# Kernel tuning notes

Measured on AMD Instinct MI355X. Metric: run time of the kernel, lower is better.

## Reference

```python
import jax, jax.numpy as jnp
import numpy as np
from jax import lax

B = 4; NB = 8192; N = B * NB; C = 64; K = 32; S = 128
GRID = np.array([[4.0, 4.0, 4.0], [16.0, 16.0, 16.0], [2.0, 2.0, 2.0]], np.float32)
relu = jax.nn.relu
sig = jax.nn.sigmoid

def _bn(x, g, b):
    # BatchNorm1d, training mode (biased batch stats), eps=1e-5
    m = x.mean(0)
    v = jnp.var(x, axis=0)
    return (x - m) * lax.rsqrt(v + 1e-5) * g + b

def _seg_sum(x, seg):
    return jax.ops.segment_sum(x, seg, num_segments=N)

def _seg_mean(x, seg):
    s = _seg_sum(x, seg)
    cnt = _seg_sum(jnp.ones((x.shape[0], 1), x.dtype), seg)
    return s / jnp.maximum(cnt, 1.0)

def _knn_geom(pts):
    # pts: [NB,3]. cdist + KNN + per-point 3x3 PCA (linearity) + density.
    sq = (pts * pts).sum(-1)
    d = jnp.sqrt(jnp.maximum(sq[:, None] + sq[None, :] - 2.0 * (pts @ pts.T), 0.0))
    negd, idx = lax.top_k(-d, K + 1)
    idx = idx[:, 1:]          # drop self
    nd = -negd[:, 1:]         # neighbor distances [NB,K]
    nbr = pts[idx]            # [NB,K,3]
    cen = nbr - nbr.mean(1, keepdims=True)
    cov = jnp.einsum('nki,nkj->nij', cen, cen) / (K - 1)
    s = jnp.linalg.svd(cov, compute_uv=False)   # [NB,3] descending
    s = s / s.sum(-1, keepdims=True)
    lin = s[:, 0] - s[:, 1] - s[:, 2]
    dens = 1.0 / (nd.mean(1) + 1e-6)
    return lin, dens

def _cluster(coordf, batch, size):
    # torch_geometric voxel_grid (start = per-dim min) + unique(return_inverse)
    v = jnp.floor((coordf - coordf.min(0)) / jnp.maximum(size, 1e-6)).astype(jnp.int32)
    rows = jnp.concatenate([batch[:, None], v], axis=1)
    _, inv = jnp.unique(rows, axis=0, size=N, return_inverse=True, fill_value=0)
    return jnp.reshape(inv, (-1,))

def _subm_conv(f, W, table, coords, batch):
    # SubMConv3d 3x3x3: output only at active sites; hash-table neighbor lookup.
    out = jnp.zeros((f.shape[0], W.shape[-1]), f.dtype)
    k = 0
    for dx in (-1, 0, 1):
        for dy in (-1, 0, 1):
            for dz in (-1, 0, 1):
                nc = coords + jnp.array([dx, dy, dz], jnp.int32)
                valid = jnp.all((nc >= 0) & (nc < S), axis=1)
                ncc = jnp.clip(nc, 0, S - 1)
                nidx = table[batch, ncc[:, 0], ncc[:, 1], ncc[:, 2]]
                ok = valid & (nidx >= 0)
                nf = jnp.where(ok[:, None], f[jnp.maximum(nidx, 0)], 0.0)
                out = out + nf @ W[k]
                k += 1
    return out

def _forward(feat, cm_fp_w, cm_fp_b, cm_fp_g, cm_fp_beta, cm_ca_w1, cm_ca_b1, cm_ca_w2, cm_ca_b2, cm_na_w1, cm_na_b1, cm_na_w2, cm_na_b2, cm_ff_w1, cm_ff_b1, cm_ff_g, cm_ff_beta, cm_ff_w2, cm_ff_b2, cm_sa_w1, cm_sa_b1, cm_sa_w2, cm_sa_b2, fj_w1, fj_b1, fj_g, fj_beta, fj_w2, fj_b2, proj_w, proj_g, proj_beta, lw_w, lw_g, lw_beta, wt_w, adp_w, fuse_w, fuse_g, fuse_beta, conv1_w, bn1_g, bn1_b, conv2_w, bn2_g, bn2_b, coords, batch):
    # ---- CMPFE ----
    p = relu(_bn(feat @ cm_fp_w + cm_fp_b, cm_fp_g, cm_fp_beta))
    cf, colf, nof = p[:, 0:3], p[:, 3:6], p[:, 6:9]
    ca = sig(relu(colf @ cm_ca_w1 + cm_ca_b1) @ cm_ca_w2 + cm_ca_b2)
    na = sig(relu(nof @ cm_na_w1 + cm_na_b1) @ cm_na_w2 + cm_na_b2)
    enh = jnp.concatenate([cf, colf * ca, nof * na], axis=1)
    ff = relu(_bn(enh @ cm_ff_w1 + cm_ff_b1, cm_ff_g, cm_ff_beta)) @ cm_ff_w2 + cm_ff_b2
    sa = sig(relu(ff @ cm_sa_w1 + cm_sa_b1) @ cm_sa_w2 + cm_sa_b2)
    feat = ff * sa + feat * (1.0 - sa)

    # ---- PFAS: geometry (per scene, sequential to bound memory) ----
    coordf = coords.astype(feat.dtype)
    lin, dens = lax.map(_knn_geom, coordf.reshape(B, NB, 3))
    lin = lin.reshape(-1)
    dens = dens.reshape(-1)

    logits = relu(_bn(feat @ fj_w1 + fj_b1, fj_g, fj_beta)) @ fj_w2 + fj_b2
    probs = jax.nn.softmax(logits, axis=1)
    tower = (2.0 * dens + probs[:, 0]) / 3.0
    back = (jnp.maximum(1.0 - lin, 1.0 - dens) + probs[:, 1]) / 3.0
    line = (2.0 * lin + probs[:, 2]) / 3.0
    opts = jnp.asarray(GRID)
    lg = opts[2] * jnp.array([1.0, 1.0, 5.0], feat.dtype)  # z grid x5 for lines
    gs = tower[:, None] * opts[0] + back[:, None] * opts[1] + line[:, None] * lg + 1e-6

    # ---- representative grids (N > 200 branch) ----
    gm = gs.mean(1)
    order = jnp.argsort(gm)
    reps = [gs[order[100:200]].mean(0), gs[order[::-1][:100]].mean(0), gs[order[:100]].mean(0)]

    # ---- multi-depth cluster attention fusion ----
    feats = []
    for i in range(3):
        cl = _cluster(coordf, batch, reps[i])
        pw = relu(_bn(feat @ lw_w[i], lw_g[i], lw_beta[i]))
        pw = pw - _seg_mean(pw, cl)[cl]
        pw = pw @ wt_w[i]
        pw = jnp.exp(pw - jnp.max(pw))
        pw = pw / (_seg_sum(pw, cl)[cl] + 1e-6)
        pf = relu(_bn(feat @ proj_w[i], proj_g[i], proj_beta[i])) * pw
        feats.append(_seg_sum(pf, cl)[cl])
    adp = jax.nn.softmax(feat @ adp_w, axis=1)           # [N,3]
    fused = jnp.einsum('nc,ncd->nd', adp, jnp.stack(feats, axis=1))
    fl = relu(_bn(feat @ proj_w[3], proj_g[3], proj_beta[3]))
    h = relu(_bn(jnp.concatenate([fl, fused], axis=1) @ fuse_w, fuse_g, fuse_beta)) + feat
    res = h

    # ---- sparse voxel residual block ----
    table = jnp.full((B, S, S, S), -1, jnp.int32).at[batch, coords[:, 0], coords[:, 1], coords[:, 2]].set(jnp.arange(N, dtype=jnp.int32))
    v = relu(_bn(_subm_conv(h, conv1_w, table, coords, batch), bn1_g, bn1_b))
    v = _bn(_subm_conv(v, conv2_w, table, coords, batch), bn2_g, bn2_b)
    return relu(v + res)

def setup_inputs() -> dict:
    key = jax.random.key(0)
    ks = iter(jax.random.split(key, 80))
    rng = np.random.default_rng(0)
    cl = []
    for b in range(B):  # unique voxel coords per scene
        li = rng.choice(S ** 3, size=NB, replace=False)
        cl.append(np.stack([li // (S * S), (li // S) % S, li % S], axis=1))
    coords = jnp.asarray(np.concatenate(cl, 0), jnp.int32)
    batch = jnp.repeat(jnp.arange(B, dtype=jnp.int32), NB)

    def W(sh, fan):
        return jax.random.normal(next(ks), sh, jnp.float32) / np.sqrt(fan)

    def bias(sh):
        return 0.01 * jax.random.normal(next(ks), sh, jnp.float32)

    def gamma(sh):
        return 1.0 + 0.01 * jax.random.normal(next(ks), sh, jnp.float32)

    inp = dict(
        feat=jax.random.normal(next(ks), (N, C), jnp.float32),
        coords=coords, batch=batch,
        cm_fp_w=W((C, 9), C), cm_fp_b=bias((9,)), cm_fp_g=gamma((9,)), cm_fp_beta=bias((9,)),
        cm_ca_w1=W((3, 16), 3), cm_ca_b1=bias((16,)), cm_ca_w2=W((16, 3), 16), cm_ca_b2=bias((3,)),
        cm_na_w1=W((3, 16), 3), cm_na_b1=bias((16,)), cm_na_w2=W((16, 3), 16), cm_na_b2=bias((3,)),
        cm_ff_w1=W((9, C), 9), cm_ff_b1=bias((C,)), cm_ff_g=gamma((C,)), cm_ff_beta=bias((C,)),
        cm_ff_w2=W((C, C), C), cm_ff_b2=bias((C,)),
        cm_sa_w1=W((C, C // 2), C), cm_sa_b1=bias((C // 2,)), cm_sa_w2=W((C // 2, 1), C // 2), cm_sa_b2=bias((1,)),
        fj_w1=W((C, 64), C), fj_b1=bias((64,)), fj_g=gamma((64,)), fj_beta=bias((64,)),
        fj_w2=W((64, 3), 64), fj_b2=bias((3,)),
        proj_w=W((4, C, C), C), proj_g=gamma((4, C)), proj_beta=bias((4, C)),
        lw_w=W((3, C, C), C), lw_g=gamma((3, C)), lw_beta=bias((3, C)),
        wt_w=W((3, C, C), C), adp_w=W((C, 3), C),
        fuse_w=W((2 * C, C), 2 * C), fuse_g=gamma((C,)), fuse_beta=bias((C,)),
        conv1_w=W((27, C, C), 27 * C), bn1_g=gamma((C,)), bn1_b=bias((C,)),
        conv2_w=W((27, C, C), 27 * C), bn2_g=gamma((C,)), bn2_b=bias((C,)))
    return inp

def reference(feat, coords, batch, cm_fp_w, cm_fp_b, cm_fp_g, cm_fp_beta, cm_ca_w1, cm_ca_b1, cm_ca_w2, cm_ca_b2, cm_na_w1, cm_na_b1, cm_na_w2, cm_na_b2, cm_ff_w1, cm_ff_b1, cm_ff_g, cm_ff_beta, cm_ff_w2, cm_ff_b2, cm_sa_w1, cm_sa_b1, cm_sa_w2, cm_sa_b2, fj_w1, fj_b1, fj_g, fj_beta, fj_w2, fj_b2, proj_w, proj_g, proj_beta, lw_w, lw_g, lw_beta, wt_w, adp_w, fuse_w, fuse_g, fuse_beta, conv1_w, bn1_g, bn1_b, conv2_w, bn2_g, bn2_b):
    return _forward(feat, cm_fp_w, cm_fp_b, cm_fp_g, cm_fp_beta, cm_ca_w1, cm_ca_b1, cm_ca_w2, cm_ca_b2, cm_na_w1, cm_na_b1, cm_na_w2, cm_na_b2, cm_ff_w1, cm_ff_b1, cm_ff_g, cm_ff_beta, cm_ff_w2, cm_ff_b2, cm_sa_w1, cm_sa_b1, cm_sa_w2, cm_sa_b2, fj_w1, fj_b1, fj_g, fj_beta, fj_w2, fj_b2, proj_w, proj_g, proj_beta, lw_w, lw_g, lw_beta, wt_w, adp_w, fuse_w, fuse_g, fuse_beta, conv1_w, bn1_g, bn1_b, conv2_w, bn2_g, bn2_b, coords, batch)
```

## Files before the change

kernel.cpp:

```cpp
#include <hip/hip_runtime.h>

typedef unsigned int u32;
typedef unsigned long long u64;
typedef unsigned short u16;

#define NPTS 32768
#define NBP 8192
#define SD 128
#define KP1 33
#define NSPLIT 4
#define NROWS (NSPLIT*KP1)
#define HCAP (1u<<18)
#define MB8 8388608ULL
#define DCAP 136
#define DSTR 138
#define KCAP 57

__device__ __forceinline__ float fsig(float x){ return 1.0f/(1.0f+expf(-x)); }
__device__ __forceinline__ u32 f2o(float f){ u32 b=__float_as_uint(f); return (b&0x80000000u)? ~b : (b|0x80000000u); }
__device__ __forceinline__ float o2f(u32 o){ u32 b=(o&0x80000000u)? (o&0x7fffffffu) : ~o; return __uint_as_float(b); }
__device__ __forceinline__ u32 hashk(u64 k){
  k^=k>>33; k*=0xff51afd7ed558ccdULL; k^=k>>33; k*=0xc4ceb9fe1a85ec53ULL; k^=k>>33;
  return (u32)k;
}
__device__ __forceinline__ void bnab(const float* st,const float* g,const float* be,int c,float& A,float& B){
  float m=st[c]*(1.0f/32768.0f);
  float var=st[64+c]*(1.0f/32768.0f)-m*m;
  var=fmaxf(var,0.f);
  float a=g[c]/sqrtf(var+1e-5f);
  A=a; B=be[c]-m*a;
}

__global__ void k_initmisc(int* misc){ int t=threadIdx.x; if(t<3) misc[t]=0x7fffffff; }

__global__ __launch_bounds__(256) void k_prep(const int* coords,int* misc,int* table){
  int t=blockIdx.x*256+threadIdx.x;
  int x=coords[3*t],y=coords[3*t+1],z=coords[3*t+2];
  int mx=x,my=y,mz=z;
  for(int o=32;o>=1;o>>=1){ mx=min(mx,__shfl_down(mx,o)); my=min(my,__shfl_down(my,o)); mz=min(mz,__shfl_down(mz,o)); }
  if((threadIdx.x&63)==0){ atomicMin(&misc[0],mx); atomicMin(&misc[1],my); atomicMin(&misc[2],mz); }
  int b=t>>13;
  table[(((b<<7)|x)<<7|y)<<7|z]=t;
}

__global__ __launch_bounds__(256) void k1(const float* feat,const float* w,const float* b,float* P9,float* st0){
  __shared__ float sm[256*17];
  __shared__ float wl[576];
  __shared__ float bl[9];
  int tid=threadIdx.x; int n0=blockIdx.x*256;
  for(int i=tid;i<576;i+=256) wl[i]=w[i];
  if(tid<9) bl[tid]=b[tid];
  float acc[9];
  #pragma unroll
  for(int c=0;c<9;c++) acc[c]=0.f;
  for(int ch=0;ch<4;ch++){
    __syncthreads();
    for(int m=0;m<16;m++){
      int e=tid+256*m; int p=e>>4,c=e&15;
      sm[p*17+c]=feat[(size_t)(n0+p)*64+ch*16+c];
    }
    __syncthreads();
    for(int j=0;j<16;j++){
      float x=sm[tid*17+j];
      const float* r=&wl[(ch*16+j)*9];
      #pragma unroll
      for(int c=0;c<9;c++) acc[c]+=x*r[c];
    }
  }
  #pragma unroll
  for(int c=0;c<9;c++) acc[c]+=bl[c];
  int n=n0+tid;
  #pragma unroll
  for(int c=0;c<9;c++) P9[(size_t)n*9+c]=acc[c];
  int lane=tid&63;
  for(int c=0;c<9;c++){
    float v=acc[c],v2=v*v;
    for(int o=32;o>=1;o>>=1){ v+=__shfl_down(v,o); v2+=__shfl_down(v2,o); }
    if(lane==0){ atomicAdd(&st0[c],v); atomicAdd(&st0[64+c],v2); }
  }
}

__global__ __launch_bounds__(256) void k2(const float* P9,const float* fpg,const float* fpbe,
    const float* caw1,const float* cab1,const float* caw2,const float* cab2,
    const float* naw1,const float* nab1,const float* naw2,const float* nab2,
    const float* ffw1,const float* ffb1,const float* st0,float* T1,float* st1){
  __shared__ float A0[9],B0[9];
  __shared__ float cw1[48],cb1[16],cw2[48],cb2[3];
  __shared__ float nw1[48],nb1[16],nw2[48],nb2[3];
  __shared__ float fw[576],fb[64];
  __shared__ float redS[256],redQ[256];
  int tid=threadIdx.x;
  if(tid<9){
    float m=st0[tid]*(1.0f/32768.0f);
    float var=st0[64+tid]*(1.0f/32768.0f)-m*m;
    var=fmaxf(var,0.f);
    float a=fpg[tid]/sqrtf(var+1e-5f);
    A0[tid]=a; B0[tid]=fpbe[tid]-m*a;
  }
  for(int i=tid;i<48;i+=256){ cw1[i]=caw1[i]; cw2[i]=caw2[i]; nw1[i]=naw1[i]; nw2[i]=naw2[i]; }
  if(tid<16){ cb1[tid]=cab1[tid]; nb1[tid]=nab1[tid]; }
  if(tid<3){ cb2[tid]=cab2[tid]; nb2[tid]=nab2[tid]; }
  for(int i=tid;i<576;i+=256) fw[i]=ffw1[i];
  if(tid<64) fb[tid]=ffb1[tid];
  __syncthreads();
  int n=blockIdx.x*256+tid;
  float p[9];
  #pragma unroll
  for(int c=0;c<9;c++){ float x=P9[(size_t)n*9+c]; p[c]=fmaxf(x*A0[c]+B0[c],0.f); }
  float ca[3],na[3];
  {
    float h[16];
    #pragma unroll
    for(int hh=0;hh<16;hh++){ float s=cb1[hh];
      #pragma unroll
      for(int c=0;c<3;c++) s+=p[3+c]*cw1[c*16+hh];
      h[hh]=fmaxf(s,0.f); }
    #pragma unroll
    for(int o=0;o<3;o++){ float s=cb2[o];
      #pragma unroll
      for(int hh=0;hh<16;hh++) s+=h[hh]*cw2[hh*3+o];
      ca[o]=fsig(s); }
  }
  {
    float h[16];
    #pragma unroll
    for(int hh=0;hh<16;hh++){ float s=nb1[hh];
      #pragma unroll
      for(int c=0;c<3;c++) s+=p[6+c]*nw1[c*16+hh];
      h[hh]=fmaxf(s,0.f); }
    #pragma unroll
    for(int o=0;o<3;o++){ float s=nb2[o];
      #pragma unroll
      for(int hh=0;hh<16;hh++) s+=h[hh]*nw2[hh*3+o];
      na[o]=fsig(s); }
  }
  float enh[9]={p[0],p[1],p[2],p[3]*ca[0],p[4]*ca[1],p[5]*ca[2],p[6]*na[0],p[7]*na[1],p[8]*na[2]};
  float acc[64];
  #pragma unroll
  for(int co=0;co<64;co++) acc[co]=fb[co];
  #pragma unroll
  for(int c=0;c<9;c++){ float x=enh[c]; const float* r=&fw[c*64];
    #pragma unroll
    for(int co=0;co<64;co++) acc[co]+=x*r[co]; }
  float4* o4=(float4*)&T1[(size_t)n*64];
  #pragma unroll
  for(int q=0;q<16;q++) o4[q]=make_float4(acc[4*q],acc[4*q+1],acc[4*q+2],acc[4*q+3]);
  int lane=tid&63, wv=tid>>6;
  for(int c=0;c<64;c++){
    float v=acc[c],v2=v*v;
    for(int o=32;o>=1;o>>=1){ v+=__shfl_down(v,o); v2+=__shfl_down(v2,o); }
    if(lane==0){ redS[wv*64+c]=v; redQ[wv*64+c]=v2; }
  }
  __syncthreads();
  if(tid<64){
    float a=0,b2=0;
    for(int w=0;w<4;w++){ a+=redS[w*64+tid]; b2+=redQ[w*64+tid]; }
    atomicAdd(&st1[tid],a); atomicAdd(&st1[64+tid],b2);
  }
}

__global__ __launch_bounds__(256) void k3(const float* T1,const float* feat,float* FF,float* T2,
    const float* st1,const float* ffg,const float* ffbe,
    const float* w2,const float* b2,
    const float* saw1,const float* sab1,const float* saw2,const float* sab2,
    const float* fjw1,const float* fjb1,float* st2){
  __shared__ float it[64*65];
  __shared__ float wt[4096];
  __shared__ float wsa[2048];
  __shared__ float red[2048];
  __shared__ float sb1[32],sw2[32],sav[64];
  __shared__ float A1[64],B1[64];
  __shared__ float sb2s;
  int tid=threadIdx.x; int n0=blockIdx.x*64;
  if(tid<64){ float A,B; bnab(st1,ffg,ffbe,tid,A,B); A1[tid]=A; B1[tid]=B; }
  for(int m=0;m<16;m++){ int i=tid+256*m; wt[i]=w2[i]; }
  for(int i=tid;i<2048;i+=256) wsa[i]=saw1[i];
  if(tid<32){ sb1[tid]=sab1[tid]; sw2[tid]=saw2[tid]; }
  if(tid==0) sb2s=sab2[0];
  __syncthreads();
  for(int m=0;m<16;m++){
    int e=tid+256*m; int p=e>>6,c=e&63;
    float x=T1[(size_t)n0*64+e];
    it[p*65+c]=fmaxf(x*A1[c]+B1[c],0.f);
  }
  __syncthreads();
  int tx4=tid&15, ty=tid>>4;
  float acc[4][4];
  #pragma unroll
  for(int j=0;j<4;j++){
    #pragma unroll
    for(int q=0;q<4;q++) acc[j][q]=0.f;
  }
  for(int ci=0;ci<64;ci++){
    float4 w4=*(float4*)&wt[ci*64+tx4*4];
    #pragma unroll
    for(int j=0;j<4;j++){
      float x=it[(ty+16*j)*65+ci];
      acc[j][0]+=x*w4.x; acc[j][1]+=x*w4.y; acc[j][2]+=x*w4.z; acc[j][3]+=x*w4.w;
    }
  }
  float bb[4];
  #pragma unroll
  for(int q=0;q<4;q++) bb[q]=b2[tx4*4+q];
  __syncthreads();
  #pragma unroll
  for(int j=0;j<4;j++){
    #pragma unroll
    for(int q=0;q<4;q++) it[(ty+16*j)*65+tx4*4+q]=acc[j][q]+bb[q];
  }
  __syncthreads();
  if(tid<64){
    float s1[32];
    #pragma unroll
    for(int h=0;h<32;h++) s1[h]=sb1[h];
    for(int ci=0;ci<64;ci++){
      float x=it[tid*65+ci];
      #pragma unroll
      for(int h=0;h<32;h++) s1[h]+=x*wsa[ci*32+h];
    }
    float s=sb2s;
    #pragma unroll
    for(int h=0;h<32;h++) s+=fmaxf(s1[h],0.f)*sw2[h];
    sav[tid]=fsig(s);
  }
  __syncthreads();
  for(int m=0;m<16;m++){
    int e=tid+256*m; int p=e>>6,c=e&63;
    float ffv=it[p*65+c]; float sv=sav[p];
    float fn=ffv*sv+feat[(size_t)n0*64+e]*(1.0f-sv);
    FF[(size_t)n0*64+e]=fn;
    it[p*65+c]=fn;
  }
  __syncthreads();
  for(int m=0;m<16;m++){ int i=tid+256*m; wt[i]=fjw1[i]; }
  __syncthreads();
  float ac2[4][4];
  #pragma unroll
  for(int j=0;j<4;j++){
    #pragma unroll
    for(int q=0;q<4;q++) ac2[j][q]=0.f;
  }
  for(int ci=0;ci<64;ci++){
    float4 w4=*(float4*)&wt[ci*64+tx4*4];
    #pragma unroll
    for(int j=0;j<4;j++){
      float x=it[(ty+16*j)*65+ci];
      ac2[j][0]+=x*w4.x; ac2[j][1]+=x*w4.y; ac2[j][2]+=x*w4.z; ac2[j][3]+=x*w4.w;
    }
  }
  float fjb[4];
  #pragma unroll
  for(int q=0;q<4;q++) fjb[q]=fjb1[tx4*4+q];
  #pragma unroll
  for(int j=0;j<4;j++){
    #pragma unroll
    for(int q=0;q<4;q++) ac2[j][q]+=fjb[q];
    *(float4*)&T2[(size_t)(n0+ty+16*j)*64+tx4*4]=make_float4(ac2[j][0],ac2[j][1],ac2[j][2],ac2[j][3]);
  }
  #pragma unroll
  for(int q=0;q<4;q++){
    float s=0,s2=0;
    #pragma unroll
    for(int j=0;j<4;j++){ s+=ac2[j][q]; s2+=ac2[j][q]*ac2[j][q]; }
    red[ty*64+tx4*4+q]=s; red[1024+ty*64+tx4*4+q]=s2;
  }
  __syncthreads();
  if(tid<64){
    float a=0,b3=0;
    for(int t=0;t<16;t++){ a+=red[t*64+tid]; b3+=red[1024+t*64+tid]; }
    atomicAdd(&st2[tid],a); atomicAdd(&st2[64+tid],b3);
  }
}

__global__ __launch_bounds__(256) void k4(const float* T2,const float* FF,const float* st2,
    const float* fjg,const float* fjbe,const float* fjw2,const float* fjb2,
    const float* adpw,float* PROBS,float* ADP){
  __shared__ float t2t[64*65],fft[64*65];
  __shared__ float A2[64],B2[64];
  __shared__ float w2l[192],b2l[3],awl[192];
  int tid=threadIdx.x; int n0=blockIdx.x*64;
  if(tid<64){ float A,B; bnab(st2,fjg,fjbe,tid,A,B); A2[tid]=A; B2[tid]=B; }
  for(int i=tid;i<192;i+=256){ w2l[i]=fjw2[i]; awl[i]=adpw[i]; }
  if(tid<3) b2l[tid]=fjb2[tid];
  for(int m=0;m<16;m++){
    int e=tid+256*m; int p=e>>6,c=e&63;
    t2t[p*65+c]=T2[(size_t)n0*64+e];
    fft[p*65+c]=FF[(size_t)n0*64+e];
  }
  __syncthreads();
  if(tid<64){
    float l0=b2l[0],l1=b2l[1],l2=b2l[2];
    float a0=0,a1=0,a2=0;
    for(int c=0;c<64;c++){
      float x=fmaxf(t2t[tid*65+c]*A2[c]+B2[c],0.f);
      l0+=x*w2l[c*3]; l1+=x*w2l[c*3+1]; l2+=x*w2l[c*3+2];
      float f=fft[tid*65+c];
      a0+=f*awl[c*3]; a1+=f*awl[c*3+1]; a2+=f*awl[c*3+2];
    }
    int n=n0+tid;
    {
      float m=fmaxf(l0,fmaxf(l1,l2));
      float e0=expf(l0-m),e1=expf(l1-m),e2=expf(l2-m);
      float s=e0+e1+e2;
      PROBS[3*n]=e0/s; PROBS[3*n+1]=e1/s; PROBS[3*n+2]=e2/s;
    }
    {
      float m=fmaxf(a0,fmaxf(a1,a2));
      float e0=expf(a0-m),e1=expf(a1-m),e2=expf(a2-m);
      float s=e0+e1+e2;
      ADP[3*n]=e0/s; ADP[3*n+1]=e1/s; ADP[3*n+2]=e2/s;
    }
  }
}

__global__ __launch_bounds__(256,2) void k5a(const int* coords,u32* PART){
  __shared__ __align__(16) u32 tile[2048];
  __shared__ u16 dl[256*DSTR];
  int tid=threadIdx.x;
  int qb=blockIdx.x>>2, s=blockIdx.x&3;
  int q=qb*256+tid;
  int base=(q>>13)*NBP;
  int cstart=s*2048;
  int qx=coords[3*q],qy=coords[3*q+1],qz=coords[3*q+2];
  for(int m=0;m<8;m++){
    int j=tid+256*m; int ci=base+cstart+j;
    tile[j]=((u32)coords[3*ci]<<14)|((u32)coords[3*ci+1]<<7)|(u32)coords[3*ci+2];
  }
  __syncthreads();
  const uint4* t4=(const uint4*)tile;

  const u32 R[6]={128u,338u,891u,2352u,6208u,16384u};
  u32 c6[6]={0,0,0,0,0,0};
  for(int j8=0;j8<256;j8++){
    uint4 a=t4[2*j8], b=t4[2*j8+1];
    u32 pcs[8]={a.x,a.y,a.z,a.w,b.x,b.y,b.z,b.w};
    #pragma unroll
    for(int e=0;e<8;e++){
      u32 pc=pcs[e];
      int dx=(int)(pc>>14)-qx, dy=(int)((pc>>7)&127)-qy, dz=(int)(pc&127)-qz;
      u32 d2=(u32)(dx*dx+dy*dy+dz*dz);
      #pragma unroll
      for(int k=0;k<6;k++) c6[k]+=(d2-R[k])>>31;
    }
  }
  u32 Tlo=1u, Thi=49153u;
  #pragma unroll
  for(int k=0;k<6;k++) if(c6[k]<33u) Tlo=R[k];
  #pragma unroll
  for(int k=5;k>=0;k--) if(c6[k]>=33u) Thi=R[k];

  int cnt=0;
  for(int rep=0;rep<8;rep++){
    cnt=0;
    for(int j8=0;j8<256;j8++){
      uint4 a=t4[2*j8], b=t4[2*j8+1];
      u32 pcs[8]={a.x,a.y,a.z,a.w,b.x,b.y,b.z,b.w};
      #pragma unroll
      for(int e=0;e<8;e++){
        u32 pc=pcs[e];
        int dx=(int)(pc>>14)-qx, dy=(int)((pc>>7)&127)-qy, dz=(int)(pc&127)-qz;
        u32 d2=(u32)(dx*dx+dy*dy+dz*dz);
        if(d2<Thi){
          if(cnt<DCAP) dl[tid*DSTR+cnt]=(u16)d2;
          cnt++;
        }
      }
    }
    bool bad=(cnt>DCAP)||(cnt<33);
    if(!__any(bad?1:0)) break;
    if(cnt>DCAP){
      if(Thi-Tlo>1u){
        float gm=sqrtf((float)Tlo*(float)Thi);
        u32 nm=(u32)gm;
        if(nm<=Tlo) nm=Tlo+1u;
        if(nm>=Thi) nm=Thi-1u;
        Thi=nm;
      }
    } else if(cnt<33){
      Tlo=Thi;
      Thi=min(Thi*2u+64u,49153u);
    }
  }
  if(cnt>DCAP) cnt=DCAP;

  u32 lo=Tlo, hi=Thi-1u;
  for(int it=0;it<17;it++){
    if(__all((lo>=hi)?1:0)) break;
    u32 mid=lo+((hi-lo)>>1);
    u32 c=0;
    for(int x=0;x<cnt;x++){
      u32 d=dl[tid*DSTR+x];
      c+=(d-(mid+1u))>>31;
    }
    if(lo<hi){ if(c>=33u) hi=mid; else lo=mid+1u; }
  }
  u32 T=hi+1u;

  u32* kl=(u32*)dl;
  const int KS=DSTR/2;
  int c2=0;
  for(int j8=0;j8<256;j8++){
    uint4 a=t4[2*j8], b=t4[2*j8+1];
    u32 pcs[8]={a.x,a.y,a.z,a.w,b.x,b.y,b.z,b.w};
    #pragma unroll
    for(int e=0;e<8;e++){
      u32 pc=pcs[e];
      int dx=(int)(pc>>14)-qx, dy=(int)((pc>>7)&127)-qy, dz=(int)(pc&127)-qz;
      u32 d2=(u32)(dx*dx+dy*dy+dz*dz);
      if(d2<T && c2<KCAP){
        kl[tid*KS+c2]=(d2<<13)|(u32)(cstart+8*j8+e);
        c2++;
      }
    }
  }
  for(int e33=0;e33<KP1;e33++){
    u32 best=0xffffffffu; int bi=-1;
    for(int x=0;x<c2;x++){
      u32 v=kl[tid*KS+x];
      if(v<best){ best=v; bi=x; }
    }
    if(bi>=0) kl[tid*KS+bi]=0xffffffffu;
    PART[(size_t)(s*KP1+e33)*NPTS+q]=best;
  }
}

__global__ __launch_bounds__(64) void k5b(const int* coords,const u32* PART,const float* PROBS,
                                          float* GS,u32* GMU){
  __shared__ u32 lk[NROWS*64];
  int tid=threadIdx.x;
  int q=blockIdx.x*64+tid;
  int b=q>>13, base=b*NBP;
  for(int s=0;s<NROWS;s++) lk[s*64+tid]=PART[(size_t)s*NPTS+q];
  int h0=0,h1=0,h2=0,h3=0;
  float snd=0.f;
  int Sx=0,Sy=0,Sz=0,Sxx=0,Sxy=0,Sxz=0,Syy=0,Syz=0,Szz=0;
  for(int t=0;t<KP1;t++){
    u32 v0=(h0<KP1)?lk[(0*KP1+h0)*64+tid]:0xffffffffu;
    u32 v1=(h1<KP1)?lk[(1*KP1+h1)*64+tid]:0xffffffffu;
    u32 v2=(h2<KP1)?lk[(2*KP1+h2)*64+tid]:0xffffffffu;
    u32 v3=(h3<KP1)?lk[(3*KP1+h3)*64+tid]:0xffffffffu;
    u32 mk=min(min(v0,v1),min(v2,v3));
    if(mk==v0) h0++; else if(mk==v1) h1++; else if(mk==v2) h2++; else h3++;
    u32 d2=mk>>13;
    if(d2==0u) continue;
    int idx=(int)(mk&8191u)+base;
    int cx=coords[3*idx],cy=coords[3*idx+1],cz=coords[3*idx+2];
    snd+=sqrtf((float)d2);
    Sx+=cx;Sy+=cy;Sz+=cz;
    Sxx+=cx*cx;Sxy+=cx*cy;Sxz+=cx*cz;Syy+=cy*cy;Syz+=cy*cz;Szz+=cz*cz;
  }
  const double i32d=1.0/32.0;
  float c00=((float)((double)Sxx-(double)Sx*(double)Sx*i32d))/31.0f;
  float c11=((float)((double)Syy-(double)Sy*(double)Sy*i32d))/31.0f;
  float c22=((float)((double)Szz-(double)Sz*(double)Sz*i32d))/31.0f;
  float c01=((float)((double)Sxy-(double)Sx*(double)Sy*i32d))/31.0f;
  float c02=((float)((double)Sxz-(double)Sx*(double)Sz*i32d))/31.0f;
  float c12=((float)((double)Syz-(double)Sy*(double)Sz*i32d))/31.0f;
  double a=c00,bd=c11,cc=c22,d=c01,e=c02,f=c12;
  double qd=(a+bd+cc)/3.0;
  double p1=d*d+e*e+f*f;
  double p2=(a-qd)*(a-qd)+(bd-qd)*(bd-qd)+(cc-qd)*(cc-qd)+2.0*p1;
  double e0,e1,e2;
  if(p2<=1e-24){ e0=e1=e2=qd; }
  else{
    double pp=sqrt(p2/6.0);
    double inv=1.0/pp;
    double b00=(a-qd)*inv,b11=(bd-qd)*inv,b22=(cc-qd)*inv;
    double b01=d*inv,b02=e*inv,b12=f*inv;
    double det=b00*(b11*b22-b12*b12)-b01*(b01*b22-b12*b02)+b02*(b01*b12-b11*b02);
    double r=det*0.5; r=fmin(1.0,fmax(-1.0,r));
    double phi=acos(r)/3.0;
    e0=qd+2.0*pp*cos(phi);
    e2=qd+2.0*pp*cos(phi+2.0943951023931953);
    e1=3.0*qd-e0-e2;
  }
  e0=fmax(e0,0.0); e1=fmax(e1,0.0); e2=fmax(e2,0.0);
  double sum=e0+e1+e2; if(sum<1e-30) sum=1e-30;
  float lin=(float)((e0-e1-e2)/sum);
  float dens=1.0f/(snd*(1.0f/32.0f)+1e-6f);
  float p0=PROBS[3*q],p1f=PROBS[3*q+1],p2f=PROBS[3*q+2];
  float tw=(2.0f*dens+p0)/3.0f;
  float bk=(fmaxf(1.0f-lin,1.0f-dens)+p1f)/3.0f;
  float ln=(2.0f*lin+p2f)/3.0f;
  float gx=tw*4.0f+bk*16.0f+ln*2.0f+1e-6f;
  float gz=tw*4.0f+bk*16.0f+ln*10.0f+1e-6f;
  GS[3*q]=gx; GS[3*q+1]=gx; GS[3*q+2]=gz;
  float gm=((gx+gx)+gz)/3.0f;
  GMU[q]=f2o(gm);
}

__global__ __launch_bounds__(1024) void k7(const u32* GMU,u32* misc){
  __shared__ int wpart[16*16];
  int tid=threadIdx.x; int lane=tid&63, wv=tid>>6;
  u32 uv[32];
  for(int m=0;m<32;m++) uv[m]=GMU[tid+1024*m];
  const int kt[6]={0,99,100,199,32668,32767};
  u32 lo[6],hi[6];
  #pragma unroll
  for(int t=0;t<6;t++){ lo[t]=0u; hi[t]=0xffffffffu; }
  for(int it=0;it<32;it++){
    u32 mid[6]; int cnt[6];
    #pragma unroll
    for(int t=0;t<6;t++){ mid[t]=lo[t]+((hi[t]-lo[t])>>1); cnt[t]=0; }
    for(int m=0;m<32;m++){
      u32 u=uv[m];
      #pragma unroll
      for(int t=0;t<6;t++) cnt[t]+=(u<=mid[t])?1:0;
    }
    #pragma unroll
    for(int t=0;t<6;t++) for(int o=32;o>=1;o>>=1) cnt[t]+=__shfl_down(cnt[t],o);
    if(lane==0){
      #pragma unroll
      for(int t=0;t<6;t++) wpart[wv*16+t]=cnt[t];
    }
    __syncthreads();
    #pragma unroll
    for(int t=0;t<6;t++){
      int s=0;
      for(int w=0;w<16;w++) s+=wpart[w*16+t];
      if(lo[t]<hi[t]){ if(s>=kt[t]+1) hi[t]=mid[t]; else lo[t]=mid[t]+1; }
    }
    __syncthreads();
  }
  int clt[6],cle[6];
  #pragma unroll
  for(int t=0;t<6;t++){ clt[t]=0; cle[t]=0; }
  for(int m=0;m<32;m++){
    u32 u=uv[m];
    #pragma unroll
    for(int t=0;t<6;t++){ clt[t]+=(u<lo[t])?1:0; cle[t]+=(u<=lo[t])?1:0; }
  }
  #pragma unroll
  for(int t=0;t<6;t++) for(int o=32;o>=1;o>>=1){ clt[t]+=__shfl_down(clt[t],o); cle[t]+=__shfl_down(cle[t],o); }
  if(lane==0){
    #pragma unroll
    for(int t=0;t<6;t++){ wpart[wv*16+t]=clt[t]; wpart[wv*16+8+t]=cle[t]; }
  }
  __syncthreads();
  if(tid==0){
    int CLT[6],CLE[6];
    for(int t=0;t<6;t++){
      int s1=0,s2=0;
      for(int w=0;w<16;w++){ s1+=wpart[w*16+t]; s2+=wpart[w*16+8+t]; }
      CLT[t]=s1; CLE[t]=s2;
    }
    const int wa[3]={100,0,32668}, wb[3]={200,100,32768};
    const int tl[3]={2,0,4}, th[3]={3,1,5};
    for(int w=0;w<3;w++){
      u32 ulo=lo[tl[w]], uhi=lo[th[w]];
      int A=wa[w],Bv=wb[w];
      int ql,qh;
      if(ulo==uhi){ ql=Bv-A; qh=0; }
      else{
        ql=min(CLE[tl[w]],Bv)-max(CLT[tl[w]],A);
        qh=min(CLE[th[w]],Bv)-max(CLT[th[w]],A);
      }
      misc[16+8*w]=ulo; misc[17+8*w]=uhi; misc[18+8*w]=(u32)ql; misc[19+8*w]=(u32)qh;
    }
  }
}

__global__ __launch_bounds__(256) void k8(const u32* GMU,const float* GS,u32* misc){
  int n=blockIdx.x*256+threadIdx.x;
  u32 u=GMU[n];
  float* rep=(float*)&misc[48];
  for(int w=0;w<3;w++){
    u32 ulo=misc[16+8*w],uhi=misc[17+8*w];
    int ql=(int)misc[18+8*w],qh=(int)misc[19+8*w];
    bool mem=false;
    if(ulo==uhi){ if(u==ulo) mem=((int)atomicAdd(&misc[40+2*w],1u)<ql); }
    else if(u>ulo&&u<uhi) mem=true;
    else if(u==ulo) mem=((int)atomicAdd(&misc[40+2*w],1u)<ql);
    else if(u==uhi) mem=((int)atomicAdd(&misc[41+2*w],1u)<qh);
    if(mem){
      atomicAdd(&rep[3*w],GS[3*n]);
      atomicAdd(&rep[3*w+1],GS[3*n+1]);
      atomicAdd(&rep[3*w+2],GS[3*n+2]);
    }
  }
}

__device__ __forceinline__ u64 clkey(int n,int i,const int* coords,const u32* misc){
  const float* rep=(const float*)&misc[48];
  const int* cmin=(const int*)misc;
  int w=(i==0)?0:((i==1)?2:1);
  u64 key=((u64)i<<62)|((u64)(n>>13)<<60);
  #pragma unroll
  for(int c=0;c<3;c++){
    float sz=fmaxf(rep[3*w+c]/100.0f,1e-6f);
    float v=floorf(((float)(coords[3*n+c]-cmin[c]))/sz);
    u32 vi=(u32)fminf(v,1048575.0f);
    key|=((u64)vi)<<(40-20*c);
  }
  return key;
}

__global__ __launch_bounds__(256) void k9a(const int* coords,u32* misc,u64* HK,int* HV){
  int n=blockIdx.x*256+threadIdx.x;
  for(int i=0;i<3;i++){
    u64 key=clkey(n,i,coords,misc);
    u32 h=hashk(key)&(HCAP-1);
    for(;;){
      u64 old=atomicCAS(&HK[h],0xffffffffffffffffULL,key);
      if(old==0xffffffffffffffffULL){
        int id=(int)atomicAdd(&misc[4+i],1u);
        HV[h]=id;
        break;
      }
      if(old==key) break;
      h=(h+1)&(HCAP-1);
    }
  }
}

__global__ __launch_bounds__(256) void k9b(const int* coords,const u32* misc,const u64* HK,const int* HV,int* CL){
  int n=blockIdx.x*256+threadIdx.x;
  for(int i=0;i<3;i++){
    u64 key=clkey(n,i,coords,misc);
    u32 h=hashk(key)&(HCAP-1);
    while(HK[h]!=key) h=(h+1)&(HCAP-1);
    CL[i*NPTS+n]=HV[h];
  }
}

__global__ __launch_bounds__(256) void k_mm(const float* IN,const float* W,const float* bias,
                                            float* OUT,float* stats,u32* gmx){
  __shared__ float it[64*65];
  __shared__ float wt[4096];
  __shared__ float red[2048];
  int tid=threadIdx.x; int n0=blockIdx.x*64;
  for(int m=0;m<16;m++){ int e=tid+256*m; it[(e>>6)*65+(e&63)]=IN[(size_t)n0*64+e]; }
  for(int m=0;m<16;m++){ int i=tid+256*m; wt[i]=W[i]; }
  __syncthreads();
  int tx4=tid&15, ty=tid>>4;
  float acc[4][4];
  #pragma unroll
  for(int j=0;j<4;j++){
    #pragma unroll
    for(int q=0;q<4;q++) acc[j][q]=0.f;
  }
  for(int ci=0;ci<64;ci++){
    float4 w4=*(float4*)&wt[ci*64+tx4*4];
    #pragma unroll
    for(int j=0;j<4;j++){
      float x=it[(ty+16*j)*65+ci];
      acc[j][0]+=x*w4.x; acc[j][1]+=x*w4.y; acc[j][2]+=x*w4.z; acc[j][3]+=x*w4.w;
    }
  }
  if(bias){
    float b0=bias[tx4*4],b1=bias[tx4*4+1],b2=bias[tx4*4+2],b3=bias[tx4*4+3];
    #pragma unroll
    for(int j=0;j<4;j++){ acc[j][0]+=b0; acc[j][1]+=b1; acc[j][2]+=b2; acc[j][3]+=b3; }
  }
  #pragma unroll
  for(int j=0;j<4;j++)
    *(float4*)&OUT[(size_t)(n0+ty+16*j)*64+tx4*4]=make_float4(acc[j][0],acc[j][1],acc[j][2],acc[j][3]);
  if(stats){
    #pragma unroll
    for(int q=0;q<4;q++){
      float s=0,s2=0;
      #pragma unroll
      for(int j=0;j<4;j++){ s+=acc[j][q]; s2+=acc[j][q]*acc[j][q]; }
      red[ty*64+tx4*4+q]=s; red[1024+ty*64+tx4*4+q]=s2;
    }
    __syncthreads();
    if(tid<64){
      float a=0,b=0;
      for(int t=0;t<16;t++){ a+=red[t*64+tid]; b+=red[1024+t*64+tid]; }
      atomicAdd(&stats[tid],a); atomicAdd(&stats[64+tid],b);
    }
  }
  if(gmx){
    float mx=acc[0][0];
    #pragma unroll
    for(int j=0;j<4;j++){
      #pragma unroll
      for(int q=0;q<4;q++) mx=fmaxf(mx,acc[j][q]);
    }
    for(int o=32;o>=1;o>>=1) mx=fmaxf(mx,__shfl_down(mx,o));
    if((tid&63)==0) red[1536+(tid>>6)]=mx;
    __syncthreads();
    if(tid==0){
      float m2=fmaxf(fmaxf(red[1536],red[1537]),fmaxf(red[1538],red[1539]));
      atomicMax(gmx,f2o(m2));
    }
  }
}

__global__ __launch_bounds__(256) void k_conv(const float* IN,const float* W27,const int* coords,
                                              const int* table,float* OUT,float* stats){
  __shared__ float nf[64*65];
  __shared__ float wt[4096];
  __shared__ float red[2048];
  __shared__ int nid[27*64];
  int tid=threadIdx.x; int n0=blockIdx.x*64;
  if(tid<64){
    int n=n0+tid;
    int x=coords[3*n],y=coords[3*n+1],z=coords[3*n+2];
    int b=n>>13;
    for(int k=0;k<27;k++){
      int dx=k/9-1,dy=(k/3)%3-1,dz=k%3-1;
      int nx=x+dx,ny=y+dy,nz=z+dz;
      int id=-1;
      if(nx>=0&&nx<SD&&ny>=0&&ny<SD&&nz>=0&&nz<SD) id=table[(((b<<7)|nx)<<7|ny)<<7|nz];
      nid[k*64+tid]=id;
    }
  }
  int tx4=tid&15, ty=tid>>4;
  float acc[4][4];
  #pragma unroll
  for(int j=0;j<4;j++){
    #pragma unroll
    for(int q=0;q<4;q++) acc[j][q]=0.f;
  }
  for(int k=0;k<27;k++){
    __syncthreads();
    for(int m=0;m<16;m++){ int i=tid+256*m; wt[i]=W27[(size_t)k*4096+i]; }
    for(int m=0;m<16;m++){
      int e=tid+256*m; int p=e>>6,c=e&63;
      int id=nid[k*64+p];
      nf[p*65+c]=(id>=0)?IN[(size_t)id*64+c]:0.0f;
    }
    __syncthreads();
    for(int ci=0;ci<64;ci++){
      float4 w4=*(float4*)&wt[ci*64+tx4*4];
      #pragma unroll
      for(int j=0;j<4;j++){
        float x=nf[(ty+16*j)*65+ci];
        acc[j][0]+=x*w4.x; acc[j][1]+=x*w4.y; acc[j][2]+=x*w4.z; acc[j][3]+=x*w4.w;
      }
    }
  }
  #pragma unroll
  for(int j=0;j<4;j++)
    *(float4*)&OUT[(size_t)(n0+ty+16*j)*64+tx4*4]=make_float4(acc[j][0],acc[j][1],acc[j][2],acc[j][3]);
  #pragma unroll
  for(int q=0;q<4;q++){
    float s=0,s2=0;
    #pragma unroll
    for(int j=0;j<4;j++){ s+=acc[j][q]; s2+=acc[j][q]*acc[j][q]; }
    red[ty*64+tx4*4+q]=s; red[1024+ty*64+tx4*4+q]=s2;
  }
  __syncthreads();
  if(tid<64){
    float a=0,b=0;
    for(int t=0;t<16;t++){ a+=red[t*64+tid]; b+=red[1024+t*64+tid]; }
    atomicAdd(&stats[tid],a); atomicAdd(&stats[64+tid],b);
  }
}

__global__ __launch_bounds__(256) void k10b(const float* T1,const int* CL,const float* st,
    const float* g,const float* be,float* SEGA,int* CNT){
  int e=blockIdx.x*256+threadIdx.x; int n=e>>6,c=e&63;
  int cl=CL[n];
  float A,B; bnab(st,g,be,c,A,B);
  float pw=fmaxf(T1[e]*A+B,0.f);
  atomicAdd(&SEGA[(size_t)cl*64+c],pw);
  if(c==0) atomicAdd(&CNT[cl],1);
}

__global__ __launch_bounds__(256) void k10c1(const float* T1,const int* CL,const float* st,
    const float* g,const float* be,const float* SEGA,const int* CNT,float* T2){
  int e=blockIdx.x*256+threadIdx.x; int n=e>>6,c=e&63;
  int cl=CL[n];
  float A,B; bnab(st,g,be,c,A,B);
  float pw=fmaxf(T1[e]*A+B,0.f);
  float mean=SEGA[(size_t)cl*64+c]/fmaxf((float)CNT[cl],1.0f);
  T2[e]=pw-mean;
}

__global__ __launch_bounds__(256) void k10d(float* T1,const int* CL,const u32* gmx,float* SEGB){
  int e=blockIdx.x*256+threadIdx.x; int n=e>>6,c=e&63;
  int cl=CL[n];
  float gm=o2f(*gmx);
  float v=expf(T1[e]-gm);
  T1[e]=v;
  atomicAdd(&SEGB[(size_t)cl*64+c],v);
}

__global__ __launch_bounds__(256) void k10f(const float* T2,const float* T1,const int* CL,
    const float* st,const float* g,const float* be,const float* SEGB,float* SEGA){
  int e=blockIdx.x*256+threadIdx.x; int n=e>>6,c=e&63;
  int cl=CL[n];
  float A,B; bnab(st,g,be,c,A,B);
  float pf=fmaxf(T2[e]*A+B,0.f);
  float pw=T1[e]/(SEGB[(size_t)cl*64+c]+1e-6f);
  atomicAdd(&SEGA[(size_t)cl*64+c],pf*pw);
}

__global__ __launch_bounds__(256) void k10g(const float* SEGA,const int* CL,const float* ADP,int i,float* FUSED){
  int e=blockIdx.x*256+threadIdx.x; int n=e>>6,c=e&63;
  int cl=CL[n];
  FUSED[e]+=ADP[3*n+i]*SEGA[(size_t)cl*64+c];
}

__global__ __launch_bounds__(256) void k12(const float* T1,const float* FUSED,const float* fw,
    const float* st9,const float* g9,const float* be9,float* T2,float* st10){
  __shared__ float it[64*129];
  __shared__ float red[2048];
  __shared__ float A9[64],B9[64];
  int tid=threadIdx.x; int n0=blockIdx.x*64;
  if(tid<64){ float A,B; bnab(st9,g9,be9,tid,A,B); A9[tid]=A; B9[tid]=B; }
  __syncthreads();
  for(int m=0;m<16;m++){
    int e=tid+256*m; int p=e>>6,c=e&63;
    float x=T1[(size_t)n0*64+e];
    it[p*129+c]=fmaxf(x*A9[c]+B9[c],0.f);
  }
  for(int m=0;m<16;m++){
    int e=tid+256*m; int p=e>>6,c=e&63;
    it[p*129+64+c]=FUSED[(size_t)n0*64+e];
  }
  __syncthreads();
  int tx4=tid&15, ty=tid>>4;
  float acc[4][4];
  #pragma unroll
  for(int j=0;j<4;j++){
    #pragma unroll
    for(int q=0;q<4;q++) acc[j][q]=0.f;
  }
  for(int ci=0;ci<128;ci++){
    float4 w4=*(const float4*)&fw[ci*64+tx4*4];
    #pragma unroll
    for(int j=0;j<4;j++){
      float x=it[(ty+16*j)*129+ci];
      acc[j][0]+=x*w4.x; acc[j][1]+=x*w4.y; acc[j][2]+=x*w4.z; acc[j][3]+=x*w4.w;
    }
  }
  #pragma unroll
  for(int j=0;j<4;j++)
    *(float4*)&T2[(size_t)(n0+ty+16*j)*64+tx4*4]=make_float4(acc[j][0],acc[j][1],acc[j][2],acc[j][3]);
  #pragma unroll
  for(int q=0;q<4;q++){
    float s=0,s2=0;
    #pragma unroll
    for(int j=0;j<4;j++){ s+=acc[j][q]; s2+=acc[j][q]*acc[j][q]; }
    red[ty*64+tx4*4+q]=s; red[1024+ty*64+tx4*4+q]=s2;
  }
  __syncthreads();
  if(tid<64){
    float a=0,b=0;
    for(int t=0;t<16;t++){ a+=red[t*64+tid]; b+=red[1024+t*64+tid]; }
    atomicAdd(&st10[tid],a); atomicAdd(&st10[64+tid],b);
  }
}

__global__ __launch_bounds__(256) void k13(const float* T2,const float* FF,const float* st,
    const float* g,const float* be,float* H){
  int e=blockIdx.x*256+threadIdx.x; int c=e&63;
  float A,B; bnab(st,g,be,c,A,B);
  H[e]=fmaxf(T2[e]*A+B,0.f)+FF[e];
}

__global__ __launch_bounds__(256) void k15(float* T1,const float* st,const float* g,const float* be){
  int e=blockIdx.x*256+threadIdx.x; int c=e&63;
  float A,B; bnab(st,g,be,c,A,B);
  T1[e]=fmaxf(T1[e]*A+B,0.f);
}

__global__ __launch_bounds__(256) void k17(const float* T2,const float* H,const float* st,
    const float* g,const float* be,float* OUT){
  int e=blockIdx.x*256+threadIdx.x; int c=e&63;
  float A,B; bnab(st,g,be,c,A,B);
  float v=fmaxf(T2[e]*A+B+H[e],0.f);
  OUT[e]=v;
}

extern "C" void kernel_launch(void* const* d_in,const int* in_sizes,int n_in,
                              void* d_out,int out_size,void* d_ws,size_t ws_size,
                              hipStream_t stream){
  (void)in_sizes;(void)n_in;(void)out_size;(void)ws_size;
  const float* feat   =(const float*)d_in[0];
  const int* coords   =(const int*)d_in[1];
  const float* cm_fp_w  =(const float*)d_in[3];
  const float* cm_fp_b  =(const float*)d_in[4];
  const float* cm_fp_g  =(const float*)d_in[5];
  const float* cm_fp_be =(const float*)d_in[6];
  const float* cm_ca_w1 =(const float*)d_in[7];
  const float* cm_ca_b1 =(const float*)d_in[8];
  const float* cm_ca_w2 =(const float*)d_in[9];
  const float* cm_ca_b2 =(const float*)d_in[10];
  const float* cm_na_w1 =(const float*)d_in[11];
  const float* cm_na_b1 =(const float*)d_in[12];
  const float* cm_na_w2 =(const float*)d_in[13];
  const float* cm_na_b2 =(const float*)d_in[14];
  const float* cm_ff_w1 =(const float*)d_in[15];
  const float* cm_ff_b1 =(const float*)d_in[16];
  const float* cm_ff_g  =(const float*)d_in[17];
  const float* cm_ff_be =(const float*)d_in[18];
  const float* cm_ff_w2 =(const float*)d_in[19];
  const float* cm_ff_b2 =(const float*)d_in[20];
  const float* cm_sa_w1 =(const float*)d_in[21];
  const float* cm_sa_b1 =(const float*)d_in[22];
  const float* cm_sa_w2 =(const float*)d_in[23];
  const float* cm_sa_b2 =(const float*)d_in[24];
  const float* fj_w1    =(const float*)d_in[25];
  const float* fj_b1    =(const float*)d_in[26];
  const float* fj_g     =(const float*)d_in[27];
  const float* fj_be    =(const float*)d_in[28];
  const float* fj_w2    =(const float*)d_in[29];
  const float* fj_b2    =(const float*)d_in[30];
  const float* proj_w   =(const float*)d_in[31];
  const float* proj_g   =(const float*)d_in[32];
  const float* proj_be  =(const float*)d_in[33];
  const float* lw_w     =(const float*)d_in[34];
  const float* lw_g     =(const float*)d_in[35];
  const float* lw_be    =(const float*)d_in[36];
  const float* wt_w     =(const float*)d_in[37];
  const float* adp_w    =(const float*)d_in[38];
  const float* fuse_w   =(const float*)d_in[39];
  const float* fuse_g   =(const float*)d_in[40];
  const float* fuse_be  =(const float*)d_in[41];
  const float* conv1_w  =(const float*)d_in[42];
  const float* bn1_g    =(const float*)d_in[43];
  const float* bn1_b    =(const float*)d_in[44];
  const float* conv2_w  =(const float*)d_in[45];
  const float* bn2_g    =(const float*)d_in[46];
  const float* bn2_b    =(const float*)d_in[47];

  char* ws=(char*)d_ws;
  const size_t OFF_H=0, OFF_R2=MB8, OFF_T1=2*MB8, OFF_T2=3*MB8, OFF_FF=4*MB8,
               OFF_SEGA=5*MB8, OFF_SEGB=6*MB8, OFF_TABLE=7*MB8;
  const size_t OFF_CL   =OFF_TABLE+33554432ULL;
  const size_t OFF_CNT  =OFF_CL+393216ULL;
  const size_t OFF_HKEY =OFF_CNT+131072ULL;
  const size_t OFF_HVAL =OFF_HKEY+2097152ULL;
  const size_t OFF_PROBS=OFF_HVAL+1048576ULL;
  const size_t OFF_GS   =OFF_PROBS+393216ULL;
  const size_t OFF_GMU  =OFF_GS+393216ULL;
  const size_t OFF_ADP  =OFF_GMU+131072ULL;
  const size_t OFF_STATS=OFF_ADP+393216ULL;
  const size_t OFF_MISC =OFF_STATS+8192ULL;

  float* H    =(float*)(ws+OFF_H);
  float* P9   =(float*)(ws+OFF_R2);
  float* FUSED=(float*)(ws+OFF_R2);
  float* T1   =(float*)(ws+OFF_T1);
  float* T2   =(float*)(ws+OFF_T2);
  float* FF   =(float*)(ws+OFF_FF);
  float* SEGA =(float*)(ws+OFF_SEGA);
  float* SEGB =(float*)(ws+OFF_SEGB);
  u32*   PART =(u32*)  (ws+OFF_H);
  int*   TABLE=(int*)  (ws+OFF_TABLE);
  int*   CL   =(int*)  (ws+OFF_CL);
  int*   CNT  =(int*)  (ws+OFF_CNT);
  u64*   HKEY =(u64*)  (ws+OFF_HKEY);
  int*   HVAL =(int*)  (ws+OFF_HVAL);
  float* PROBS=(float*)(ws+OFF_PROBS);
  float* GS   =(float*)(ws+OFF_GS);
  u32*   GMU  =(u32*)  (ws+OFF_GMU);
  float* ADP  =(float*)(ws+OFF_ADP);
  float* STATS=(float*)(ws+OFF_STATS);
  u32*   MISCu=(u32*)  (ws+OFF_MISC);
  int*   MISCi=(int*)  (ws+OFF_MISC);
  u32*   GMX  =MISCu+8;
  #define ST(s) (STATS+(s)*128)

  hipMemsetAsync(ws+OFF_STATS,0,9216,stream);
  hipMemsetAsync(ws+OFF_HKEY,0xFF,(size_t)HCAP*8,stream);
  k_initmisc<<<1,64,0,stream>>>(MISCi);
  k_prep<<<128,256,0,stream>>>(coords,MISCi,TABLE);

  k1<<<128,256,0,stream>>>(feat,cm_fp_w,cm_fp_b,P9,ST(0));
  k2<<<128,256,0,stream>>>(P9,cm_fp_g,cm_fp_be,cm_ca_w1,cm_ca_b1,cm_ca_w2,cm_ca_b2,
                           cm_na_w1,cm_na_b1,cm_na_w2,cm_na_b2,cm_ff_w1,cm_ff_b1,ST(0),T1,ST(1));
  k3<<<512,256,0,stream>>>(T1,feat,FF,T2,ST(1),cm_ff_g,cm_ff_be,cm_ff_w2,cm_ff_b2,
                           cm_sa_w1,cm_sa_b1,cm_sa_w2,cm_sa_b2,fj_w1,fj_b1,ST(2));
  k4<<<512,256,0,stream>>>(T2,FF,ST(2),fj_g,fj_be,fj_w2,fj_b2,adp_w,PROBS,ADP);

  k5a<<<512,256,0,stream>>>(coords,PART);
  k5b<<<512,64,0,stream>>>(coords,PART,PROBS,GS,GMU);
  k7<<<1,1024,0,stream>>>(GMU,MISCu);
  k8<<<128,256,0,stream>>>(GMU,GS,MISCu);
  k9a<<<128,256,0,stream>>>(coords,MISCu,HKEY,HVAL);
  k9b<<<128,256,0,stream>>>(coords,MISCu,HKEY,HVAL,CL);

  hipMemsetAsync(ws+OFF_R2,0,MB8,stream);
  for(int i=0;i<3;i++){
    hipMemsetAsync(ws+OFF_SEGA,0,MB8,stream);
    hipMemsetAsync(ws+OFF_CNT,0,131072,stream);
    k_mm<<<512,256,0,stream>>>(FF,lw_w+(size_t)i*4096,(const float*)nullptr,T1,ST(3+i),(u32*)nullptr);
    k10b<<<8192,256,0,stream>>>(T1,CL+i*NPTS,ST(3+i),lw_g+i*64,lw_be+i*64,SEGA,CNT);
    k10c1<<<8192,256,0,stream>>>(T1,CL+i*NPTS,ST(3+i),lw_g+i*64,lw_be+i*64,SEGA,CNT,T2);
    k_mm<<<512,256,0,stream>>>(T2,wt_w+(size_t)i*4096,(const float*)nullptr,T1,(float*)nullptr,GMX+i);
    hipMemsetAsync(ws+OFF_SEGB,0,MB8,stream);
    k10d<<<8192,256,0,stream>>>(T1,CL+i*NPTS,GMX+i,SEGB);
    k_mm<<<512,256,0,stream>>>(FF,proj_w+(size_t)i*4096,(const float*)nullptr,T2,ST(6+i),(u32*)nullptr);
    hipMemsetAsync(ws+OFF_SEGA,0,MB8,stream);
    k10f<<<8192,256,0,stream>>>(T2,T1,CL+i*NPTS,ST(6+i),proj_g+i*64,proj_be+i*64,SEGB,SEGA);
    k10g<<<8192,256,0,stream>>>(SEGA,CL+i*NPTS,ADP,i,FUSED);
  }

  k_mm<<<512,256,0,stream>>>(FF,proj_w+(size_t)3*4096,(const float*)nullptr,T1,ST(9),(u32*)nullptr);
  k12<<<512,256,0,stream>>>(T1,FUSED,fuse_w,ST(9),proj_g+192,proj_be+192,T2,ST(10));
  k13<<<8192,256,0,stream>>>(T2,FF,ST(10),fuse_g,fuse_be,H);

  k_conv<<<512,256,0,stream>>>(H,conv1_w,coords,TABLE,T1,ST(11));
  k15<<<8192,256,0,stream>>>(T1,ST(11),bn1_g,bn1_b);
  k_conv<<<512,256,0,stream>>>(T1,conv2_w,coords,TABLE,T2,ST(12));
  k17<<<8192,256,0,stream>>>(T2,H,ST(12),bn2_g,bn2_b,(float*)d_out);
}
```

Baseline: 1.990 ms.

## Replace iterative KNN threshold search with power-of-two histogram and quartile refinement

```diff
diff --git a/kernel.cpp b/kernel.cpp
--- a/kernel.cpp
+++ b/kernel.cpp
@@ -14,7 +14,7 @@
 #define MB8 8388608ULL
 #define DCAP 136
 #define DSTR 138
-#define KCAP 57
+#define KS 69
 
 __device__ __forceinline__ float fsig(float x){ return 1.0f/(1.0f+expf(-x)); }
 __device__ __forceinline__ u32 f2o(float f){ u32 b=__float_as_uint(f); return (b&0x80000000u)? ~b : (b|0x80000000u); }
@@ -329,8 +329,7 @@
   __syncthreads();
   const uint4* t4=(const uint4*)tile;
 
-  const u32 R[6]={128u,338u,891u,2352u,6208u,16384u};
-  u32 c6[6]={0,0,0,0,0,0};
+  u64 hA=0ull, hB=0ull;
   for(int j8=0;j8<256;j8++){
     uint4 a=t4[2*j8], b=t4[2*j8+1];
     u32 pcs[8]={a.x,a.y,a.z,a.w,b.x,b.y,b.z,b.w};
@@ -339,52 +338,65 @@
       u32 pc=pcs[e];
       int dx=(int)(pc>>14)-qx, dy=(int)((pc>>7)&127)-qy, dz=(int)(pc&127)-qz;
       u32 d2=(u32)(dx*dx+dy*dy+dz*dz);
-      #pragma unroll
-      for(int k=0;k<6;k++) c6[k]+=(d2-R[k])>>31;
-    }
-  }
-  u32 Tlo=1u, Thi=49153u;
-  #pragma unroll
-  for(int k=0;k<6;k++) if(c6[k]<33u) Tlo=R[k];
-  #pragma unroll
-  for(int k=5;k>=0;k--) if(c6[k]>=33u) Thi=R[k];
-
-  int cnt=0;
-  for(int rep=0;rep<8;rep++){
-    cnt=0;
-    for(int j8=0;j8<256;j8++){
-      uint4 a=t4[2*j8], b=t4[2*j8+1];
-      u32 pcs[8]={a.x,a.y,a.z,a.w,b.x,b.y,b.z,b.w};
-      #pragma unroll
-      for(int e=0;e<8;e++){
-        u32 pc=pcs[e];
-        int dx=(int)(pc>>14)-qx, dy=(int)((pc>>7)&127)-qy, dz=(int)(pc&127)-qz;
-        u32 d2=(u32)(dx*dx+dy*dy+dz*dz);
-        if(d2<Thi){
-          if(cnt<DCAP) dl[tid*DSTR+cnt]=(u16)d2;
-          cnt++;
+      u32 i=31u-(u32)__builtin_clz(d2|1u);
+      u64 inc=1ull<<((i&7u)<<3);
+      u64 ia=(i<8u)?inc:0ull;
+      hA+=ia; hB+=(inc-ia);
+    }
+  }
+  u32 cum=0u, Bi=16u, myc=0u;
+  #pragma unroll
+  for(int i=0;i<16;i++){
+    u32 ci=(u32)(((i<8)?hA:hB)>>((i&7)*8))&0xffu;
+    cum+=ci;
+    if(cum>=33u&&Bi==16u){ Bi=(u32)i; myc=cum; }
+  }
+  u32 Tlo=1u<<Bi, Thi=(Bi>=16u)?49153u:(1u<<(Bi+1));
+  for(int rr=0;rr<2;rr++){
+    if(!__any((myc>DCAP)?1:0)) break;
+    u32 g=(Thi-Tlo)>>2;
+    if(myc>DCAP&&g>0u){
+      u32 m1=Tlo+g,m2=Tlo+2u*g,m3=Tlo+3u*g;
+      u32 c1=0,c2c=0,c3=0;
+      for(int j8=0;j8<256;j8++){
+        uint4 a=t4[2*j8], b=t4[2*j8+1];
+        u32 pcs[8]={a.x,a.y,a.z,a.w,b.x,b.y,b.z,b.w};
+        #pragma unroll
+        for(int e=0;e<8;e++){
+          u32 pc=pcs[e];
+          int dx=(int)(pc>>14)-qx, dy=(int)((pc>>7)&127)-qy, dz=(int)(pc&127)-qz;
+          u32 d2=(u32)(dx*dx+dy*dy+dz*dz);
+          c1+=(d2-m1)>>31; c2c+=(d2-m2)>>31; c3+=(d2-m3)>>31;
         }
       }
-    }
-    bool bad=(cnt>DCAP)||(cnt<33);
-    if(!__any(bad?1:0)) break;
-    if(cnt>DCAP){
-      if(Thi-Tlo>1u){
-        float gm=sqrtf((float)Tlo*(float)Thi);
-        u32 nm=(u32)gm;
-        if(nm<=Tlo) nm=Tlo+1u;
-        if(nm>=Thi) nm=Thi-1u;
-        Thi=nm;
+      if(c1>=33u){ Thi=m1; myc=c1; }
+      else if(c2c>=33u){ Tlo=m1; Thi=m2; myc=c2c; }
+      else if(c3>=33u){ Tlo=m2; Thi=m3; myc=c3; }
+      else { Tlo=m3; }
+    } else {
+      for(int j8=0;j8<0;j8++){}
+    }
+  }
+
+  int cnt=0;
+  for(int j8=0;j8<256;j8++){
+    uint4 a=t4[2*j8], b=t4[2*j8+1];
+    u32 pcs[8]={a.x,a.y,a.z,a.w,b.x,b.y,b.z,b.w};
+    #pragma unroll
+    for(int e=0;e<8;e++){
+      u32 pc=pcs[e];
+      int dx=(int)(pc>>14)-qx, dy=(int)((pc>>7)&127)-qy, dz=(int)(pc&127)-qz;
+      u32 d2=(u32)(dx*dx+dy*dy+dz*dz);
+      if(d2<Thi){
+        if(cnt<DCAP) dl[tid*DSTR+cnt]=(u16)d2;
+        cnt++;
       }
-    } else if(cnt<33){
-      Tlo=Thi;
-      Thi=min(Thi*2u+64u,49153u);
     }
   }
   if(cnt>DCAP) cnt=DCAP;
 
   u32 lo=Tlo, hi=Thi-1u;
-  for(int it=0;it<17;it++){
+  for(int it=0;it<15;it++){
     if(__all((lo>=hi)?1:0)) break;
     u32 mid=lo+((hi-lo)>>1);
     u32 c=0;
@@ -397,7 +409,6 @@
   u32 T=hi+1u;
 
   u32* kl=(u32*)dl;
-  const int KS=DSTR/2;
   int c2=0;
   for(int j8=0;j8<256;j8++){
     uint4 a=t4[2*j8], b=t4[2*j8+1];
@@ -407,7 +418,7 @@
       u32 pc=pcs[e];
       int dx=(int)(pc>>14)-qx, dy=(int)((pc>>7)&127)-qy, dz=(int)(pc&127)-qz;
       u32 d2=(u32)(dx*dx+dy*dy+dz*dz);
-      if(d2<T && c2<KCAP){
+      if(d2<T && c2<KS){
         kl[tid*KS+c2]=(d2<<13)|(u32)(cstart+8*j8+e);
         c2++;
       }
@@ -977,13 +988,12 @@
 
   hipMemsetAsync(ws+OFF_R2,0,MB8,stream);
   for(int i=0;i<3;i++){
-    hipMemsetAsync(ws+OFF_SEGA,0,MB8,stream);
+    hipMemsetAsync(ws+OFF_SEGA,0,2*MB8,stream);
     hipMemsetAsync(ws+OFF_CNT,0,131072,stream);
     k_mm<<<512,256,0,stream>>>(FF,lw_w+(size_t)i*4096,(const float*)nullptr,T1,ST(3+i),(u32*)nullptr);
     k10b<<<8192,256,0,stream>>>(T1,CL+i*NPTS,ST(3+i),lw_g+i*64,lw_be+i*64,SEGA,CNT);
     k10c1<<<8192,256,0,stream>>>(T1,CL+i*NPTS,ST(3+i),lw_g+i*64,lw_be+i*64,SEGA,CNT,T2);
     k_mm<<<512,256,0,stream>>>(T2,wt_w+(size_t)i*4096,(const float*)nullptr,T1,(float*)nullptr,GMX+i);
-    hipMemsetAsync(ws+OFF_SEGB,0,MB8,stream);
     k10d<<<8192,256,0,stream>>>(T1,CL+i*NPTS,GMX+i,SEGB);
     k_mm<<<512,256,0,stream>>>(FF,proj_w+(size_t)i*4096,(const float*)nullptr,T2,ST(6+i),(u32*)nullptr);
     hipMemsetAsync(ws+OFF_SEGA,0,MB8,stream);
```

Measured after the change: 1.874 ms. 5.8% less time.
